# Kernel tuning notes

Measured on AMD Instinct MI355X. Metric: run time of the kernel, lower is better.

## Reference

```python
import jax, jax.numpy as jnp
import numpy as np
from jax import lax

T, B, F = 512, 256, 258
IN, H = 256, 1024


def setup_inputs() -> dict:
    key = jax.random.key(0)
    ks = jax.random.split(key, 6)

    def lin_w(k, fi, fo):
        return jax.random.normal(k, (fi, fo), jnp.float32) * (1.0 / np.sqrt(fi))

    return {
        "u": jax.random.normal(ks[0], (T, B, F), jnp.float32),
        "a": jnp.float32(0.92),
        "b": jnp.float32(-0.3),
        "W0": lin_w(ks[1], IN, H), "b0": jnp.zeros((H,), jnp.float32),
        "W1": lin_w(ks[2], H, H), "b1": jnp.zeros((H,), jnp.float32),
        "W2": lin_w(ks[3], H, H), "b2": jnp.zeros((H,), jnp.float32),
        "W3": lin_w(ks[4], H, 1), "b3": jnp.zeros((1,), jnp.float32),
    }


def reference(u, a, b, W0, b0, W1, b1, W2, b2, W3, b3):
    Tn, Bn, Fn = u.shape
    # MLP over cols 2: — independent of the recurrent state, so batch all timesteps.
    feats = u[:, :, 2:].reshape(Tn * Bn, Fn - 2)
    h = jax.nn.relu(feats @ W0 + b0)
    h = jax.nn.relu(h @ W1 + b1)
    h = jax.nn.relu(h @ W2 + b2)
    net = (h @ W3 + b3).reshape(Tn, Bn)  # [T, B]

    c1 = u[:, :, 1]  # [T, B], multiplied by b each step
    y0 = u[0, :, 0]  # u_y[0]; also the col-0 value used at j=0

    def step(carry, xs):
        net_j, c1_j = xs
        y = a * carry + b * c1_j + net_j
        return y, y

    _, ys = lax.scan(step, y0, (net, c1))  # ys: [T, B] = u_y[1:]
    return jnp.concatenate([y0[None, :], ys], axis=0)  # [T+1, B]
```

## Files before the change

### kernel.cpp

```cpp
#include <hip/hip_runtime.h>
#include <hip/hip_fp16.h>

typedef _Float16 v8h __attribute__((ext_vector_type(8)));
typedef _Float16 v4h __attribute__((ext_vector_type(4)));
typedef float v4f __attribute__((ext_vector_type(4)));

#define T_DIM 512
#define B_DIM 256
#define F_DIM 258
#define IN_DIM 256
#define H_DIM 1024
#define M_ROWS (T_DIM * B_DIM)

__device__ __forceinline__ void tile_map(int b, int nM, int nN, int& mt, int& nt) {
    if ((nM & 7) == 0) {
        int xcd = b & 7;
        int l = b >> 3;
        int mpx = nM >> 3;
        int lm = l / nN;
        mt = xcd * mpx + lm;
        nt = l - lm * nN;
    } else {
        int lm = b / nN;
        mt = lm;
        nt = b - lm * nN;
    }
}

__device__ __forceinline__ void gl16(const _Float16* g, _Float16* l) {
    __builtin_amdgcn_global_load_lds(
        (const __attribute__((address_space(1))) unsigned int*)g,
        (__attribute__((address_space(3))) unsigned int*)l, 16, 0, 0);
}


__global__ void prep_x_kernel(const float* __restrict__ u,
                              _Float16* __restrict__ X, int nrows) {
    int i = blockIdx.x * blockDim.x + threadIdx.x;
    int total = nrows * 32;
    int stride = gridDim.x * blockDim.x;
    for (; i < total; i += stride) {
        int r = ((i >> 9) << 4) + (i & 15);
        int kb = (i >> 4) & 31;
        const float* s = u + (size_t)r * 258 + 2 + kb * 8;
        _Float16 h[8];
#pragma unroll
        for (int j = 0; j < 8; ++j) h[j] = (_Float16)s[j];
        *(v8h*)(X + ((size_t)(r >> 4) * 32 + kb) * 128 + (r & 15) * 8) =
            *(v8h*)h;
    }
}

__global__ void prep_c1_kernel(const float* __restrict__ u,
                               float* __restrict__ c1, int nrows) {
    int r = blockIdx.x * blockDim.x + threadIdx.x;
    if (r < nrows) c1[r] = u[(size_t)r * 258 + 1];
}

__global__ void wt_frag_kernel(const float* __restrict__ W,
                               _Float16* __restrict__ BF, int K, int N) {
    int idx = blockIdx.x * blockDim.x + threadIdx.x;
    int total = (N >> 6) * (K >> 5) * 4 * 64;
    if (idx >= total) return;
    int l = idx & 63;
    int f = idx >> 6;
    int i = f & 3;
    int gk = f >> 2;
    int KC = K >> 5;
    int g = gk / KC, kc = gk - g * KC;
    int col = g * 64 + i * 16 + (l & 15);
    int krow = kc * 32 + (l >> 4) * 8;
    _Float16 tmp[8];
#pragma unroll
    for (int j = 0; j < 8; ++j) tmp[j] = (_Float16)W[(size_t)(krow + j) * N + col];
    *(v8h*)&BF[(size_t)idx * 8] = *(v8h*)tmp;
}

__global__ void wt_vec_kernel(const float* __restrict__ W,
                              _Float16* __restrict__ Wh, int K) {
    int i = blockIdx.x * blockDim.x + threadIdx.x;
    if (i < K) Wh[i] = (_Float16)W[i];
}

__global__ void zero_kernel(float* __restrict__ p, int n) {
    int i = blockIdx.x * blockDim.x + threadIdx.x;
    if (i < n) p[i] = 0.f;
}

template <int MI0>
__device__ __forceinline__ void mfma16(v4f (&acc)[8][4], const v8h (&af)[4],
                                       const v8h (&b)[4]) {
#pragma unroll
    for (int mi = 0; mi < 4; ++mi)
#pragma unroll
        for (int ni = 0; ni < 4; ++ni)
            acc[MI0 + mi][ni] = __builtin_amdgcn_mfma_f32_16x16x32_f16(
                af[ni], b[mi], acc[MI0 + mi][ni], 0, 0, 0);
}

template <int DOT>
__global__ __launch_bounds__(256, 2)
void gemm256(const _Float16* __restrict__ Xb, const _Float16* __restrict__ WF,
             const float* __restrict__ bias, const _Float16* __restrict__ w3,
             _Float16* __restrict__ Cb, float* __restrict__ net,
             int M, int N, int K) {
    extern __shared__ _Float16 lds[];
    const int tid = threadIdx.x;
    const int lane = tid & 63;
    const int wave = tid >> 6;
    const int wm = wave >> 1;
    const int wn = wave & 1;
    const int quad = lane >> 4;
    const int r16 = lane & 15;
    const int wm8 = wm * 8;
    const int lrb = lane * 8;

    int mt, nt;
    tile_map(blockIdx.x, M >> 8, N >> 7, mt, nt);
    const int m0 = mt * 256;
    const int n0 = nt * 128;

    const int KC = K >> 5;
    const int KC8 = K >> 3;
    const int NT = KC;
    const int m016 = m0 >> 4;
    const int nt2 = nt * 2;

    auto stageA = [&](int g, int kt, _Float16* pa) {
        gl16(WF + ((size_t)(nt2 + g) * KC + kt) * 2048 + tid * 8,
             pa + g * 2048 + tid * 8);
    };
    auto stageB = [&](int mb, int kt, _Float16* pb) {
        gl16(Xb + ((size_t)(m016 + mb + (tid >> 6)) * KC8 + (size_t)kt * 4) * 128 +
                 (tid & 63) * 8,
             pb + mb * 512 + tid * 8);
    };
    auto loadB4 = [&](const _Float16* pB, int mb, v8h (&b)[4]) {
#pragma unroll
        for (int j = 0; j < 4; ++j)
            b[j] = *(const v8h*)(pB + (mb + j) * 512 + lrb);
    };

    v4f acc[8][4];
#pragma unroll
    for (int i = 0; i < 8; ++i)
#pragma unroll
        for (int j = 0; j < 4; ++j) acc[i][j] = (v4f)0.f;

    {
        _Float16* A0 = lds;
        _Float16* B0 = lds + 4096;
        stageB(0, 0, B0); stageB(4, 0, B0); stageB(8, 0, B0); stageB(12, 0, B0);
        stageA(0, 0, A0); stageA(1, 0, A0);
        asm volatile("s_waitcnt vmcnt(0)" ::: "memory");
        __builtin_amdgcn_s_barrier();
    }

#pragma unroll 2
    for (int kt = 0; kt < NT; ++kt) {
        _Float16* pAc = lds + (kt & 1) * 12288;
        _Float16* pBc = pAc + 4096;
        _Float16* pAn = lds + ((kt + 1) & 1) * 12288;
        _Float16* pBn = pAn + 4096;
        const bool pre = (kt + 1 < NT);
        const int kn = kt + 1;

        v8h af[4];
#pragma unroll
        for (int i = 0; i < 4; ++i)
            af[i] = *(const v8h*)(pAc + wn * 2048 + i * 512 + lrb);
        v8h bA[4], bB[4];
        loadB4(pBc, wm8 + 0, bA);

        if (pre) {
            stageB(0, kn, pBn); stageB(4, kn, pBn);
            stageB(8, kn, pBn); stageB(12, kn, pBn);
            stageA(0, kn, pAn); stageA(1, kn, pAn);
        }

        loadB4(pBc, wm8 + 4, bB);

        __builtin_amdgcn_s_setprio(1);
        mfma16<0>(acc, af, bA);
        __builtin_amdgcn_s_setprio(0);
        __builtin_amdgcn_s_setprio(1);
        mfma16<4>(acc, af, bB);
        __builtin_amdgcn_s_setprio(0);

        if (kt != NT - 1) {
            asm volatile("s_waitcnt vmcnt(0)" ::: "memory");
            __builtin_amdgcn_s_barrier();
        }
    }

    const int nb = n0 + wn * 64;
    v4f bv[4];
#pragma unroll
    for (int ni = 0; ni < 4; ++ni)
        bv[ni] = *(const v4f*)&bias[nb + ni * 16 + quad * 4];

    if constexpr (DOT == 0) {
        const int NC8 = N >> 3;
#pragma unroll
        for (int ni = 0; ni < 4; ++ni) {
            const int nblk = ((nb + ni * 16) >> 3) + (quad >> 1);
#pragma unroll
            for (int mi = 0; mi < 8; ++mi) {
                v4h hv;
#pragma unroll
                for (int i = 0; i < 4; ++i)
                    hv[i] = (_Float16)fmaxf(acc[mi][ni][i] + bv[ni][i], 0.f);
                const size_t mblk = (size_t)((m0 + wm * 128 + mi * 16) >> 4);
                _Float16* dst =
                    Cb + (mblk * NC8 + nblk) * 128 + r16 * 8 + (quad & 1) * 4;
                *(v4h*)dst = hv;
            }
        }
    } else {
        v4h wv[4];
#pragma unroll
        for (int ni = 0; ni < 4; ++ni)
            wv[ni] = *(const v4h*)&w3[nb + ni * 16 + quad * 4];
#pragma unroll
        for (int mi = 0; mi < 8; ++mi) {
            float t = 0.f;
#pragma unroll
            for (int ni = 0; ni < 4; ++ni)
#pragma unroll
                for (int i = 0; i < 4; ++i) {
                    float v = fmaxf(acc[mi][ni][i] + bv[ni][i], 0.f);
                    t = fmaf(v, (float)wv[ni][i], t);
                }
            t += __shfl_xor(t, 16);
            t += __shfl_xor(t, 32);
            if (quad == 0) {
                int row = m0 + wm * 128 + mi * 16 + r16;
                atomicAdd(&net[row], t);
            }
        }
    }
}

__global__ void scan_kernel(const float* __restrict__ net,
                            const float* __restrict__ c1,
                            const float* __restrict__ u,
                            const float* __restrict__ pa,
                            const float* __restrict__ pb,
                            const float* __restrict__ pb3,
                            float* __restrict__ out) {
    const int bidx = threadIdx.x;
    const float a = pa[0];
    const float b = pb[0];
    const float b3 = pb3[0];
    float y = u[(size_t)bidx * F_DIM];
    out[bidx] = y;
#pragma unroll 8
    for (int t = 0; t < T_DIM; ++t) {
        float z = fmaf(b, c1[t * B_DIM + bidx], net[t * B_DIM + bidx] + b3);
        y = fmaf(a, y, z);
        out[(t + 1) * B_DIM + bidx] = y;
    }
}

extern "C" void kernel_launch(void* const* d_in, const int* in_sizes, int n_in,
                              void* d_out, int out_size, void* d_ws, size_t ws_size,
                              hipStream_t stream) {
    const float* u = (const float*)d_in[0];
    const float* pa = (const float*)d_in[1];
    const float* pb = (const float*)d_in[2];
    const float* W0 = (const float*)d_in[3];
    const float* b0 = (const float*)d_in[4];
    const float* W1 = (const float*)d_in[5];
    const float* b1 = (const float*)d_in[6];
    const float* W2 = (const float*)d_in[7];
    const float* b2 = (const float*)d_in[8];
    const float* W3 = (const float*)d_in[9];
    const float* b3 = (const float*)d_in[10];
    float* out = (float*)d_out;

    char* ws = (char*)d_ws;
    size_t off = 0;
    auto alloc = [&](size_t bytes) -> void* {
        void* p = ws + off;
        off += (bytes + 255) & ~(size_t)255;
        return p;
    };

    float* net = (float*)alloc((size_t)M_ROWS * 4);
    float* c1 = (float*)alloc((size_t)M_ROWS * 4);
    _Float16* W0F = (_Float16*)alloc((size_t)IN_DIM * H_DIM * 2);
    _Float16* W1F = (_Float16*)alloc((size_t)H_DIM * H_DIM * 2);
    _Float16* W2F = (_Float16*)alloc((size_t)H_DIM * H_DIM * 2);
    _Float16* W3h = (_Float16*)alloc((size_t)H_DIM * 2);

    const size_t per_row = 512 + 2048 + 2048;
    size_t avail = (ws_size > off + 65536) ? (ws_size - off - 65536) : 0;
    long Rl = (long)(avail / per_row);
    Rl = (Rl / 2048) * 2048;
    if (Rl < 2048) Rl = 2048;
    if (Rl > M_ROWS) Rl = M_ROWS;
    const int R = (int)Rl;

    _Float16* Xc = (_Float16*)alloc((size_t)R * IN_DIM * 2);
    _Float16* HAc = (_Float16*)alloc((size_t)R * H_DIM * 2);
    _Float16* HBc = (_Float16*)alloc((size_t)R * H_DIM * 2);

    wt_frag_kernel<<<(IN_DIM / 32) * (H_DIM / 64), 256, 0, stream>>>(W0, W0F,
                                                                     IN_DIM, H_DIM);
    wt_frag_kernel<<<(H_DIM / 32) * (H_DIM / 64), 256, 0, stream>>>(W1, W1F,
                                                                    H_DIM, H_DIM);
    wt_frag_kernel<<<(H_DIM / 32) * (H_DIM / 64), 256, 0, stream>>>(W2, W2F,
                                                                    H_DIM, H_DIM);
    wt_vec_kernel<<<4, 256, 0, stream>>>(W3, W3h, H_DIM);
    zero_kernel<<<M_ROWS / 256, 256, 0, stream>>>(net, M_ROWS);

    const size_t lds_bytes = 49152;
    for (int r0 = 0; r0 < M_ROWS; r0 += R) {
        int Mc = M_ROWS - r0;
        if (Mc > R) Mc = R;

        int pgrid = (Mc * 32 + 255) / 256;
        if (pgrid > 2048) pgrid = 2048;
        prep_x_kernel<<<pgrid, 256, 0, stream>>>(u + (size_t)r0 * F_DIM, Xc, Mc);
        prep_c1_kernel<<<(Mc + 255) / 256, 256, 0, stream>>>(
            u + (size_t)r0 * F_DIM, c1 + r0, Mc);

        dim3 blk(256);
        dim3 grd((Mc / 256) * (H_DIM / 128));
        gemm256<0><<<grd, blk, lds_bytes, stream>>>(Xc, W0F, b0, nullptr, HAc,
                                                    nullptr, Mc, H_DIM, IN_DIM);
        gemm256<0><<<grd, blk, lds_bytes, stream>>>(HAc, W1F, b1, nullptr, HBc,
                                                    nullptr, Mc, H_DIM, H_DIM);
        gemm256<1><<<grd, blk, lds_bytes, stream>>>(HBc, W2F, b2, W3h, nullptr,
                                                    net + r0, Mc, H_DIM, H_DIM);
    }

    scan_kernel<<<1, 256, 0, stream>>>(net, c1, u, pa, pb, b3, out);
}
```

Measured before the change: 926.5 us.

## Enlarge GEMM block tile to 256x256 with 8 waves and 64-deep K steps

The MLP GEMM kernel grows from a 256x128 tile with 4 waves to a 256x256 tile with 8 waves (2x4 wave grid). Each main-loop iteration now consumes a K slice of 64 instead of 32. Fragment loads are reorganised so B fragments are loaded once per iteration and reused across four column groups. The goal is more arithmetic per byte staged through LDS and global memory, and half as many barrier iterations. The cost is 128 KB of double-buffered LDS per block, which allows only one resident block per CU, and higher register pressure.

```diff
diff --git a/kernel.cpp b/kernel.cpp
--- a/kernel.cpp
+++ b/kernel.cpp
@@ -87,19 +87,8 @@
     if (i < n) p[i] = 0.f;
 }
 
-template <int MI0>
-__device__ __forceinline__ void mfma16(v4f (&acc)[8][4], const v8h (&af)[4],
-                                       const v8h (&b)[4]) {
-#pragma unroll
-    for (int mi = 0; mi < 4; ++mi)
-#pragma unroll
-        for (int ni = 0; ni < 4; ++ni)
-            acc[MI0 + mi][ni] = __builtin_amdgcn_mfma_f32_16x16x32_f16(
-                af[ni], b[mi], acc[MI0 + mi][ni], 0, 0, 0);
-}
-
 template <int DOT>
-__global__ __launch_bounds__(256, 2)
+__global__ __launch_bounds__(512, 2)
 void gemm256(const _Float16* __restrict__ Xb, const _Float16* __restrict__ WF,
              const float* __restrict__ bias, const _Float16* __restrict__ w3,
              _Float16* __restrict__ Cb, float* __restrict__ net,
@@ -108,37 +97,32 @@
     const int tid = threadIdx.x;
     const int lane = tid & 63;
     const int wave = tid >> 6;
-    const int wm = wave >> 1;
-    const int wn = wave & 1;
+    const int wm = wave >> 2;
+    const int wn = wave & 3;
     const int quad = lane >> 4;
     const int r16 = lane & 15;
     const int wm8 = wm * 8;
     const int lrb = lane * 8;
 
     int mt, nt;
-    tile_map(blockIdx.x, M >> 8, N >> 7, mt, nt);
+    tile_map(blockIdx.x, M >> 8, N >> 8, mt, nt);
     const int m0 = mt * 256;
-    const int n0 = nt * 128;
+    const int n0 = nt * 256;
 
     const int KC = K >> 5;
     const int KC8 = K >> 3;
-    const int NT = KC;
+    const int NT = K >> 6;
     const int m016 = m0 >> 4;
-    const int nt2 = nt * 2;
+    const int nt4 = nt * 4;
 
     auto stageA = [&](int g, int kt, _Float16* pa) {
-        gl16(WF + ((size_t)(nt2 + g) * KC + kt) * 2048 + tid * 8,
-             pa + g * 2048 + tid * 8);
+        gl16(WF + ((size_t)(nt4 + g) * KC + (size_t)kt * 2) * 2048 + tid * 8,
+             pa + g * 4096 + tid * 8);
     };
     auto stageB = [&](int mb, int kt, _Float16* pb) {
-        gl16(Xb + ((size_t)(m016 + mb + (tid >> 6)) * KC8 + (size_t)kt * 4) * 128 +
-                 (tid & 63) * 8,
-             pb + mb * 512 + tid * 8);
-    };
-    auto loadB4 = [&](const _Float16* pB, int mb, v8h (&b)[4]) {
-#pragma unroll
-        for (int j = 0; j < 4; ++j)
-            b[j] = *(const v8h*)(pB + (mb + j) * 512 + lrb);
+        gl16(Xb + ((size_t)(m016 + mb + (tid >> 7)) * KC8 + (size_t)kt * 8) * 128 +
+                 (tid & 127) * 8,
+             pb + mb * 1024 + tid * 8);
     };
 
     v4f acc[8][4];
@@ -149,45 +133,88 @@
 
     {
         _Float16* A0 = lds;
-        _Float16* B0 = lds + 4096;
+        _Float16* B0 = lds + 16384;
         stageB(0, 0, B0); stageB(4, 0, B0); stageB(8, 0, B0); stageB(12, 0, B0);
-        stageA(0, 0, A0); stageA(1, 0, A0);
+        stageA(0, 0, A0); stageA(1, 0, A0); stageA(2, 0, A0); stageA(3, 0, A0);
         asm volatile("s_waitcnt vmcnt(0)" ::: "memory");
         __builtin_amdgcn_s_barrier();
     }
 
 #pragma unroll 2
     for (int kt = 0; kt < NT; ++kt) {
-        _Float16* pAc = lds + (kt & 1) * 12288;
-        _Float16* pBc = pAc + 4096;
-        _Float16* pAn = lds + ((kt + 1) & 1) * 12288;
-        _Float16* pBn = pAn + 4096;
+        _Float16* pAc = lds + (kt & 1) * 32768;
+        _Float16* pBc = pAc + 16384;
+        _Float16* pAn = lds + ((kt + 1) & 1) * 32768;
+        _Float16* pBn = pAn + 16384;
         const bool pre = (kt + 1 < NT);
         const int kn = kt + 1;
-
-        v8h af[4];
-#pragma unroll
-        for (int i = 0; i < 4; ++i)
-            af[i] = *(const v8h*)(pAc + wn * 2048 + i * 512 + lrb);
-        v8h bA[4], bB[4];
-        loadB4(pBc, wm8 + 0, bA);
+        const _Float16* pAw = pAc + wn * 4096;
+
+        v8h afA[2], afB[2];
+        afA[0] = *(const v8h*)(pAw + lrb);
+        afA[1] = *(const v8h*)(pAw + 2048 + lrb);
+        v8h bf[8][2];
+#pragma unroll
+        for (int mi = 0; mi < 8; ++mi) {
+            bf[mi][0] = *(const v8h*)(pBc + (wm8 + mi) * 1024 + lrb);
+            bf[mi][1] = *(const v8h*)(pBc + (wm8 + mi) * 1024 + 512 + lrb);
+        }
 
         if (pre) {
             stageB(0, kn, pBn); stageB(4, kn, pBn);
             stageB(8, kn, pBn); stageB(12, kn, pBn);
             stageA(0, kn, pAn); stageA(1, kn, pAn);
-        }
-
-        loadB4(pBc, wm8 + 4, bB);
-
+            stageA(2, kn, pAn); stageA(3, kn, pAn);
+        }
+
+        afB[0] = *(const v8h*)(pAw + 512 + lrb);
+        afB[1] = *(const v8h*)(pAw + 2560 + lrb);
         __builtin_amdgcn_s_setprio(1);
-        mfma16<0>(acc, af, bA);
+#pragma unroll
+        for (int mi = 0; mi < 8; ++mi) {
+            acc[mi][0] = __builtin_amdgcn_mfma_f32_16x16x32_f16(
+                afA[0], bf[mi][0], acc[mi][0], 0, 0, 0);
+            acc[mi][0] = __builtin_amdgcn_mfma_f32_16x16x32_f16(
+                afA[1], bf[mi][1], acc[mi][0], 0, 0, 0);
+        }
         __builtin_amdgcn_s_setprio(0);
+
+        afA[0] = *(const v8h*)(pAw + 1024 + lrb);
+        afA[1] = *(const v8h*)(pAw + 3072 + lrb);
         __builtin_amdgcn_s_setprio(1);
-        mfma16<4>(acc, af, bB);
+#pragma unroll
+        for (int mi = 0; mi < 8; ++mi) {
+            acc[mi][1] = __builtin_amdgcn_mfma_f32_16x16x32_f16(
+                afB[0], bf[mi][0], acc[mi][1], 0, 0, 0);
+            acc[mi][1] = __builtin_amdgcn_mfma_f32_16x16x32_f16(
+                afB[1], bf[mi][1], acc[mi][1], 0, 0, 0);
+        }
         __builtin_amdgcn_s_setprio(0);
 
+        afB[0] = *(const v8h*)(pAw + 1536 + lrb);
+        afB[1] = *(const v8h*)(pAw + 3584 + lrb);
+        __builtin_amdgcn_s_setprio(1);
+#pragma unroll
+        for (int mi = 0; mi < 8; ++mi) {
+            acc[mi][2] = __builtin_amdgcn_mfma_f32_16x16x32_f16(
+                afA[0], bf[mi][0], acc[mi][2], 0, 0, 0);
+            acc[mi][2] = __builtin_amdgcn_mfma_f32_16x16x32_f16(
+                afA[1], bf[mi][1], acc[mi][2], 0, 0, 0);
+        }
+        __builtin_amdgcn_s_setprio(0);
+
+        __builtin_amdgcn_s_setprio(1);
+#pragma unroll
+        for (int mi = 0; mi < 8; ++mi) {
+            acc[mi][3] = __builtin_amdgcn_mfma_f32_16x16x32_f16(
+                afB[0], bf[mi][0], acc[mi][3], 0, 0, 0);
+            acc[mi][3] = __builtin_amdgcn_mfma_f32_16x16x32_f16(
+                afB[1], bf[mi][1], acc[mi][3], 0, 0, 0);
+        }
+        __builtin_amdgcn_s_setprio(0);
+
         if (kt != NT - 1) {
+            asm volatile("s_waitcnt lgkmcnt(0)" ::: "memory");
             asm volatile("s_waitcnt vmcnt(0)" ::: "memory");
             __builtin_amdgcn_s_barrier();
         }
@@ -314,7 +341,7 @@
     wt_vec_kernel<<<4, 256, 0, stream>>>(W3, W3h, H_DIM);
     zero_kernel<<<M_ROWS / 256, 256, 0, stream>>>(net, M_ROWS);
 
-    const size_t lds_bytes = 49152;
+    const size_t lds_bytes = 131072;
     for (int r0 = 0; r0 < M_ROWS; r0 += R) {
         int Mc = M_ROWS - r0;
         if (Mc > R) Mc = R;
@@ -325,8 +352,8 @@
         prep_c1_kernel<<<(Mc + 255) / 256, 256, 0, stream>>>(
             u + (size_t)r0 * F_DIM, c1 + r0, Mc);
 
-        dim3 blk(256);
-        dim3 grd((Mc / 256) * (H_DIM / 128));
+        dim3 blk(512);
+        dim3 grd((Mc / 256) * (H_DIM / 256));
         gemm256<0><<<grd, blk, lds_bytes, stream>>>(Xc, W0F, b0, nullptr, HAc,
                                                     nullptr, Mc, H_DIM, IN_DIM);
         gemm256<0><<<grd, blk, lds_bytes, stream>>>(HAc, W1F, b1, nullptr, HBc,
```

Result: no change. 917.8 us (-0.9%).
